# Kernel tuning notes

Measured on AMD Instinct MI355X. Metric: run time of the kernel, lower is better.

The kernel has to match this reference:

```python
import jax, jax.numpy as jnp
import numpy as np

B, R, C, NH, G = 32, 64, 96, 3, 8   # batch, patches_resolution, dim, heads, group(window) size
HD = C // NH                         # head dim = 32
SCALE = HD ** -0.5
HID = 4 * C                          # mlp hidden = mlp_ratio * dim


def setup_inputs() -> dict:
    key = jax.random.key(0)
    ks = jax.random.split(key, 16)
    n = jax.random.normal
    s = 0.02
    return {
        "x": n(ks[0], (B, R * R, C), jnp.float32),
        "w_qkv": n(ks[1], (C, 3 * C), jnp.float32) * s,
        "b_qkv": jnp.zeros((3 * C,), jnp.float32),
        "w_lepe": n(ks[2], (C, 1, 3, 3), jnp.float32) * s,  # depthwise conv, OIHW with groups=C
        "b_lepe": jnp.zeros((C,), jnp.float32),
        "w_proj": n(ks[3], (C, C), jnp.float32) * s,
        "b_proj": jnp.zeros((C,), jnp.float32),
        "g1": jnp.ones((C,), jnp.float32),
        "bt1": jnp.zeros((C,), jnp.float32),
        "g2": jnp.ones((C,), jnp.float32),
        "bt2": jnp.zeros((C,), jnp.float32),
        "w_fc1": n(ks[4], (C, HID), jnp.float32) * s,
        "b_fc1": jnp.zeros((HID,), jnp.float32),
        "w_fc2": n(ks[5], (HID, C), jnp.float32) * s,
        "b_fc2": jnp.zeros((C,), jnp.float32),
    }


def _ln(x, g, b):
    m = x.mean(-1, keepdims=True)
    v = ((x - m) ** 2).mean(-1, keepdims=True)
    return (x - m) * jax.lax.rsqrt(v + 1e-5) * g + b


def reference(x, w_qkv, b_qkv, w_lepe, b_lepe, w_proj, b_proj,
              g1, bt1, g2, bt2, w_fc1, b_fc1, w_fc2, b_fc2):
    Bn, L, _ = x.shape
    H = W = R
    shortcut = x
    # norm1 + SDA window partition: (B,H,W,C) -> (B*nW, G*G, C)
    h = _ln(x, g1, bt1).reshape(Bn, H // G, G, W // G, G, C)
    h = h.transpose(0, 1, 3, 2, 4, 5).reshape(-1, G * G, C)
    B_ = h.shape[0]
    qkv = (h @ w_qkv + b_qkv).reshape(B_, G * G, 3, NH, HD).transpose(2, 0, 3, 1, 4)
    q, k, v = qkv[0], qkv[1], qkv[2]            # (B_, NH, G*G, HD)
    # LePE: depthwise 3x3 conv on V viewed as (B_, C, G, G)
    vimg = v.transpose(0, 1, 3, 2).reshape(B_, C, G, G)
    lepe = jax.lax.conv_general_dilated(
        vimg, w_lepe, window_strides=(1, 1), padding='SAME',
        feature_group_count=C, dimension_numbers=('NCHW', 'OIHW', 'NCHW'))
    lepe = lepe + b_lepe[None, :, None, None]
    lepe = lepe.reshape(B_, NH, HD, G * G).transpose(0, 1, 3, 2)  # (B_, NH, G*G, HD)
    # attention (no mask registered in this block)
    attn = jax.nn.softmax((q * SCALE) @ k.transpose(0, 1, 3, 2), axis=-1)
    o = (attn @ v + lepe).transpose(0, 2, 1, 3).reshape(B_, G * G, C)
    o = o @ w_proj + b_proj
    # window reverse
    o = o.reshape(Bn, H // G, W // G, G, G, C).transpose(0, 1, 3, 2, 4, 5).reshape(Bn, L, C)
    x1 = shortcut + o
    # MLP block (exact GELU, as torch nn.GELU default)
    m = _ln(x1, g2, bt2)
    m = jax.nn.gelu(m @ w_fc1 + b_fc1, approximate=False) @ w_fc2 + b_fc2
    return (x1 + m, attn)
```

## Files before the change

### kernel.cpp

```cpp
#include <hip/hip_runtime.h>
#include <hip/hip_bf16.h>

typedef short short8 __attribute__((ext_vector_type(8)));
typedef float f32x4 __attribute__((ext_vector_type(4)));

constexpr int BDIM = 32, RDIM = 64, CDIM = 96, NH_ = 3, HD_ = 32;
constexpr int LTOK = RDIM * RDIM;
constexpr int GG = 64;
constexpr int HID = 384;
constexpr int NWIN = 2048;
constexpr float SCALE = 0.17677669529663687f;
constexpr long OUT1OFF = (long)BDIM * LTOK * CDIM;

constexpr int O_WQKVT = 0;
constexpr int O_WPROJT = 27648;
constexpr int O_WFC1T = 36864;
constexpr int O_WFC2T = 73728;
constexpr int W_TOT = 110592;

__device__ __forceinline__ unsigned short f2b(float f) {
  return __builtin_bit_cast(unsigned short, __float2bfloat16(f));
}
__device__ __forceinline__ float b2f(unsigned short u) {
  return __bfloat162float(__builtin_bit_cast(__hip_bfloat16, u));
}

__global__ void prep_weights(const float* __restrict__ wqkv,
                             const float* __restrict__ wproj,
                             const float* __restrict__ wfc1,
                             const float* __restrict__ wfc2,
                             unsigned short* __restrict__ ws) {
  int i = blockIdx.x * 256 + threadIdx.x;
  if (i >= W_TOT) return;
  float v;
  if (i < O_WPROJT) {
    int n = i / 96, k = i - n * 96;
    v = wqkv[k * 288 + n];
  } else if (i < O_WFC1T) {
    int j = i - O_WPROJT, n = j / 96, k = j - n * 96;
    v = wproj[k * 96 + n];
  } else if (i < O_WFC2T) {
    int j = i - O_WFC1T, n = j / 96, k = j - n * 96;
    v = wfc1[k * 384 + n];
  } else {
    int j = i - O_WFC2T, n = j / 384, k = j - n * 384;
    v = wfc2[k * 96 + n];
  }
  ws[i] = f2b(v);
}

__global__ __launch_bounds__(256, 2)
void attn_mfma(const float* __restrict__ x, const float* __restrict__ bqkv,
               const float* __restrict__ wlepe, const float* __restrict__ blepe,
               const float* __restrict__ bproj, const float* __restrict__ g1,
               const float* __restrict__ bt1,
               const unsigned short* __restrict__ ws, float* __restrict__ out) {
  constexpr int SA = 104;
  constexpr int SQ = 200;
  constexpr int SV = 72;
  constexpr int SP = 72;
  __shared__ __attribute__((aligned(16))) unsigned short hA[64 * SA];
  __shared__ __attribute__((aligned(16))) unsigned short qkS[64 * SQ];
  __shared__ __attribute__((aligned(16))) unsigned short vS[96 * SV];
  __shared__ __attribute__((aligned(16))) unsigned short pS[64 * SP];
  float* red = (float*)pS;

  const int tid = threadIdx.x, lane = tid & 63;
  const int wv = __builtin_amdgcn_readfirstlane(tid >> 6);
  const int w = blockIdx.x, b = w >> 6, wi = w & 63, wr = wi >> 3, wc = wi & 7;
  const long xbase = (long)b * (LTOK * CDIM);
  const int l15 = lane & 15, lk = (lane >> 4) * 8, lr = (lane >> 4) * 4;

  {
    const int tok = lane;
    const long rowbase =
        xbase + (long)((wr * 8 + (tok >> 3)) * RDIM + wc * 8 + (tok & 7)) * CDIM;
    float xv[24], s1 = 0.f, s2 = 0.f;
#pragma unroll
    for (int i = 0; i < 24; ++i) {
      float v = x[rowbase + wv * 24 + i];
      xv[i] = v; s1 += v; s2 += v * v;
    }
    red[wv * 64 + tok] = s1;
    red[256 + wv * 64 + tok] = s2;
    __syncthreads();
    float m = 0.f, vv = 0.f;
#pragma unroll
    for (int q = 0; q < 4; ++q) { m += red[q * 64 + tok]; vv += red[256 + q * 64 + tok]; }
    m *= (1.f / 96.f);
    vv = vv * (1.f / 96.f) - m * m;
    float rs = rsqrtf(vv + 1e-5f);
#pragma unroll
    for (int i = 0; i < 24; ++i) {
      int c = wv * 24 + i;
      hA[tok * SA + c] = f2b((xv[i] - m) * rs * g1[c] + bt1[c]);
    }
  }
  __syncthreads();

  {
    f32x4 acc[18];
#pragma unroll
    for (int t = 0; t < 18; ++t) acc[t] = (f32x4){0.f, 0.f, 0.f, 0.f};
    const int arow = wv * 16 + l15;
#pragma unroll
    for (int kk = 0; kk < 3; ++kk) {
      short8 a = *(const short8*)&hA[arow * SA + kk * 32 + lk];
#pragma unroll
      for (int nt = 0; nt < 18; ++nt) {
        short8 bw = *(const short8*)&ws[O_WQKVT + (nt * 16 + l15) * 96 + kk * 32 + lk];
        acc[nt] = __builtin_amdgcn_mfma_f32_16x16x32_bf16(a, bw, acc[nt], 0, 0, 0);
      }
    }
#pragma unroll
    for (int nt = 0; nt < 18; ++nt) {
      int n0 = nt * 16 + l15;
      float bias = bqkv[n0];
#pragma unroll
      for (int r = 0; r < 4; ++r) {
        int tk = wv * 16 + lr + r;
        float v = acc[nt][r] + bias;
        if (n0 < 96) qkS[tk * SQ + n0] = f2b(v * SCALE);
        else if (n0 < 192) qkS[tk * SQ + n0] = f2b(v);
        else vS[(n0 - 192) * SV + tk] = f2b(v);
      }
    }
  }
  __syncthreads();

  for (int h = 0; h < NH_; ++h) {
    f32x4 sacc[4];
#pragma unroll
    for (int t = 0; t < 4; ++t) sacc[t] = (f32x4){0.f, 0.f, 0.f, 0.f};
    short8 aq = *(const short8*)&qkS[(wv * 16 + l15) * SQ + h * 32 + lk];
#pragma unroll
    for (int nt = 0; nt < 4; ++nt) {
      short8 bk = *(const short8*)&qkS[(nt * 16 + l15) * SQ + 96 + h * 32 + lk];
      sacc[nt] = __builtin_amdgcn_mfma_f32_16x16x32_bf16(aq, bk, sacc[nt], 0, 0, 0);
    }
    float p[4][4];
#pragma unroll
    for (int r = 0; r < 4; ++r) {
      float mx = -1e30f;
#pragma unroll
      for (int nt = 0; nt < 4; ++nt) mx = fmaxf(mx, sacc[nt][r]);
#pragma unroll
      for (int s = 1; s < 16; s <<= 1) mx = fmaxf(mx, __shfl_xor(mx, s, 64));
      float sum = 0.f;
#pragma unroll
      for (int nt = 0; nt < 4; ++nt) {
        float e = __expf(sacc[nt][r] - mx);
        p[nt][r] = e; sum += e;
      }
#pragma unroll
      for (int s = 1; s < 16; s <<= 1) sum += __shfl_xor(sum, s, 64);
      float inv = 1.f / sum;
#pragma unroll
      for (int nt = 0; nt < 4; ++nt) p[nt][r] *= inv;
    }
    const long o1base = OUT1OFF + ((long)(w * NH_ + h) * GG) * GG;
#pragma unroll
    for (int nt = 0; nt < 4; ++nt) {
      int col = nt * 16 + l15;
#pragma unroll
      for (int r = 0; r < 4; ++r) {
        int row = wv * 16 + lr + r;
        out[o1base + (long)row * GG + col] = p[nt][r];
        pS[row * SP + col] = f2b(p[nt][r]);
      }
    }
    f32x4 oa[2];
    oa[0] = (f32x4){0.f, 0.f, 0.f, 0.f};
    oa[1] = (f32x4){0.f, 0.f, 0.f, 0.f};
#pragma unroll
    for (int kk = 0; kk < 2; ++kk) {
      short8 ap = *(const short8*)&pS[(wv * 16 + l15) * SP + kk * 32 + lk];
#pragma unroll
      for (int nt = 0; nt < 2; ++nt) {
        short8 bv = *(const short8*)&vS[(h * 32 + nt * 16 + l15) * SV + kk * 32 + lk];
        oa[nt] = __builtin_amdgcn_mfma_f32_16x16x32_bf16(ap, bv, oa[nt], 0, 0, 0);
      }
    }
#pragma unroll
    for (int nt = 0; nt < 2; ++nt) {
      int d = nt * 16 + l15, c = h * 32 + d;
      float lw9[9];
#pragma unroll
      for (int q = 0; q < 9; ++q) lw9[q] = wlepe[c * 9 + q];
      float lb = blepe[c];
#pragma unroll
      for (int r = 0; r < 4; ++r) {
        int tk = wv * 16 + lr + r;
        int tr_ = tk >> 3, tc_ = tk & 7;
        float a = lb;
#pragma unroll
        for (int kh = 0; kh < 3; ++kh)
#pragma unroll
          for (int kw2 = 0; kw2 < 3; ++kw2) {
            int rr = tr_ + kh - 1, cc = tc_ + kw2 - 1;
            if (rr >= 0 && rr < 8 && cc >= 0 && cc < 8)
              a += lw9[kh * 3 + kw2] * b2f(vS[c * SV + rr * 8 + cc]);
          }
        hA[tk * SA + c] = f2b(oa[nt][r] + a);
      }
    }
  }
  __syncthreads();

  {
    f32x4 pacc[6];
#pragma unroll
    for (int t = 0; t < 6; ++t) pacc[t] = (f32x4){0.f, 0.f, 0.f, 0.f};
#pragma unroll
    for (int kk = 0; kk < 3; ++kk) {
      short8 ao = *(const short8*)&hA[(wv * 16 + l15) * SA + kk * 32 + lk];
#pragma unroll
      for (int nt = 0; nt < 6; ++nt) {
        short8 bw = *(const short8*)&ws[O_WPROJT + (nt * 16 + l15) * 96 + kk * 32 + lk];
        pacc[nt] = __builtin_amdgcn_mfma_f32_16x16x32_bf16(ao, bw, pacc[nt], 0, 0, 0);
      }
    }
#pragma unroll
    for (int nt = 0; nt < 6; ++nt) {
      int ch = nt * 16 + l15;
      float bias = bproj[ch];
#pragma unroll
      for (int r = 0; r < 4; ++r) {
        int tk = wv * 16 + lr + r;
        long g = xbase + (long)((wr * 8 + (tk >> 3)) * RDIM + wc * 8 + (tk & 7)) * CDIM + ch;
        out[g] = x[g] + pacc[nt][r] + bias;
      }
    }
  }
}

__global__ __launch_bounds__(256, 2)
void mlp_mfma(const float* __restrict__ bfc1, const float* __restrict__ bfc2,
              const float* __restrict__ g2, const float* __restrict__ bt2,
              const unsigned short* __restrict__ ws, float* __restrict__ out) {
  constexpr int SB = 104, SH = 392;
  __shared__ __attribute__((aligned(16))) unsigned short hB[64 * SB];
  __shared__ __attribute__((aligned(16))) unsigned short Hs[64 * SH];
  float* red = (float*)Hs;

  const int tid = threadIdx.x, lane = tid & 63;
  const int wv = __builtin_amdgcn_readfirstlane(tid >> 6);
  const long t0 = (long)blockIdx.x * GG;
  const int l15 = lane & 15, lk = (lane >> 4) * 8, lr = (lane >> 4) * 4;

  {
    const int tok = lane;
    const long rb = (t0 + tok) * CDIM;
    float xv[24], s1 = 0.f, s2 = 0.f;
#pragma unroll
    for (int i = 0; i < 24; ++i) {
      float v = out[rb + wv * 24 + i];
      xv[i] = v; s1 += v; s2 += v * v;
    }
    red[wv * 64 + tok] = s1;
    red[256 + wv * 64 + tok] = s2;
    __syncthreads();
    float m = 0.f, vv = 0.f;
#pragma unroll
    for (int q = 0; q < 4; ++q) { m += red[q * 64 + tok]; vv += red[256 + q * 64 + tok]; }
    m *= (1.f / 96.f);
    vv = vv * (1.f / 96.f) - m * m;
    float rs = rsqrtf(vv + 1e-5f);
#pragma unroll
    for (int i = 0; i < 24; ++i) {
      int c = wv * 24 + i;
      hB[tok * SB + c] = f2b((xv[i] - m) * rs * g2[c] + bt2[c]);
    }
  }
  __syncthreads();

  for (int half = 0; half < 2; ++half) {
    f32x4 acc[12];
#pragma unroll
    for (int t = 0; t < 12; ++t) acc[t] = (f32x4){0.f, 0.f, 0.f, 0.f};
#pragma unroll
    for (int kk = 0; kk < 3; ++kk) {
      short8 a = *(const short8*)&hB[(wv * 16 + l15) * SB + kk * 32 + lk];
#pragma unroll
      for (int nt = 0; nt < 12; ++nt) {
        int n = half * 192 + nt * 16 + l15;
        short8 bw = *(const short8*)&ws[O_WFC1T + n * 96 + kk * 32 + lk];
        acc[nt] = __builtin_amdgcn_mfma_f32_16x16x32_bf16(a, bw, acc[nt], 0, 0, 0);
      }
    }
#pragma unroll
    for (int nt = 0; nt < 12; ++nt) {
      int n = half * 192 + nt * 16 + l15;
      float bias = bfc1[n];
#pragma unroll
      for (int r = 0; r < 4; ++r) {
        int tk = wv * 16 + lr + r;
        float v = acc[nt][r] + bias;
        float gl = 0.5f * v * (1.f + erff(v * 0.70710678118654752f));
        Hs[tk * SH + n] = f2b(gl);
      }
    }
  }
  __syncthreads();

  {
    f32x4 acc[6];
#pragma unroll
    for (int t = 0; t < 6; ++t) acc[t] = (f32x4){0.f, 0.f, 0.f, 0.f};
#pragma unroll
    for (int kk = 0; kk < 12; ++kk) {
      short8 a = *(const short8*)&Hs[(wv * 16 + l15) * SH + kk * 32 + lk];
#pragma unroll
      for (int nt = 0; nt < 6; ++nt) {
        short8 bw = *(const short8*)&ws[O_WFC2T + (nt * 16 + l15) * 384 + kk * 32 + lk];
        acc[nt] = __builtin_amdgcn_mfma_f32_16x16x32_bf16(a, bw, acc[nt], 0, 0, 0);
      }
    }
#pragma unroll
    for (int nt = 0; nt < 6; ++nt) {
      int ch = nt * 16 + l15;
      float bias = bfc2[ch];
#pragma unroll
      for (int r = 0; r < 4; ++r) {
        int tk = wv * 16 + lr + r;
        long g = (t0 + tk) * CDIM + ch;
        out[g] = out[g] + acc[nt][r] + bias;
      }
    }
  }
}

struct PF {
  const float *x, *w_qkv, *b_qkv, *w_lepe, *b_lepe, *w_proj, *b_proj;
  const float *g1, *bt1, *g2, *bt2, *w_fc1, *b_fc1, *w_fc2, *b_fc2;
  float* out;
};

__global__ __launch_bounds__(256, 2)
void attn_scalar(PF p) {
  constexpr int SA = 66;
  __shared__ __hip_bfloat16 bufA[CDIM * SA];
  __shared__ __hip_bfloat16 qkvT[288 * GG];
  __shared__ __hip_bfloat16 sPad[GG * SA];
  __shared__ float meanS[GG], rstdS[GG];

  const int w = blockIdx.x;
  const int b = w >> 6, wi = w & 63, wr = wi >> 3, wc = wi & 7;
  const int tid = threadIdx.x, lane = tid & 63;
  const int wv = __builtin_amdgcn_readfirstlane(tid >> 6);
  const long xbase = (long)b * (LTOK * CDIM);

  for (int k = 0; k < 24; ++k) {
    int e = tid + k * 256, wrow = e / 768, o = e - wrow * 768;
    int tir = o / 96, ch = o - tir * 96;
    long g = xbase + ((wr * 8 + wrow) * RDIM + wc * 8 + tir) * CDIM + ch;
    bufA[ch * SA + wrow * 8 + tir] = __float2bfloat16(p.x[g]);
  }
  __syncthreads();
  if (wv == 0) {
    float m = 0.f;
    for (int c = 0; c < CDIM; ++c) m += __bfloat162float(bufA[c * SA + lane]);
    m *= (1.f / CDIM);
    float var = 0.f;
    for (int c = 0; c < CDIM; ++c) {
      float d = __bfloat162float(bufA[c * SA + lane]) - m;
      var += d * d;
    }
    meanS[lane] = m;
    rstdS[lane] = rsqrtf(var * (1.f / CDIM) + 1e-5f);
  }
  __syncthreads();
  {
    float m = meanS[lane], rs = rstdS[lane];
    for (int cc = 0; cc < 24; ++cc) {
      int c = wv * 24 + cc;
      float v = __bfloat162float(bufA[c * SA + lane]);
      bufA[c * SA + lane] = __float2bfloat16((v - m) * rs * p.g1[c] + p.bt1[c]);
    }
  }
  __syncthreads();
  for (int tile = 0; tile < 2; ++tile) {
    int j0 = wv * 72 + tile * 36;
    float acc[36];
#pragma unroll
    for (int jj = 0; jj < 36; ++jj) acc[jj] = p.b_qkv[j0 + jj];
#pragma unroll 1
    for (int c = 0; c < CDIM; ++c) {
      float hv = __bfloat162float(bufA[c * SA + lane]);
#pragma unroll
      for (int jj = 0; jj < 36; ++jj) acc[jj] += hv * p.w_qkv[c * 288 + j0 + jj];
    }
#pragma unroll
    for (int jj = 0; jj < 36; ++jj)
      qkvT[(j0 + jj) * GG + lane] = __float2bfloat16(acc[jj]);
  }
  __syncthreads();
  for (int hh = 0; hh < NH_; ++hh) {
    float kreg[HD_];
#pragma unroll
    for (int d = 0; d < HD_; ++d)
      kreg[d] = __bfloat162float(qkvT[(CDIM + hh * HD_ + d) * GG + lane]);
#pragma unroll 1
    for (int r = 0; r < 16; ++r) {
      int i = wv * 16 + r;
      float acc = 0.f;
#pragma unroll
      for (int d = 0; d < HD_; ++d)
        acc += __bfloat162float(qkvT[(hh * HD_ + d) * GG + i]) * kreg[d];
      sPad[lane * SA + i] = __float2bfloat16(acc * SCALE);
    }
#pragma unroll 1
    for (int r = 0; r < 16; ++r) {
      int i = wv * 16 + r;
      float v = __bfloat162float(sPad[lane * SA + i]);
      float mx = v;
#pragma unroll
      for (int s = 32; s > 0; s >>= 1) mx = fmaxf(mx, __shfl_xor(mx, s, 64));
      float e = __expf(v - mx);
      float sum = e;
#pragma unroll
      for (int s = 32; s > 0; s >>= 1) sum += __shfl_xor(sum, s, 64);
      float rr = e / sum;
      sPad[lane * SA + i] = __float2bfloat16(rr);
      p.out[OUT1OFF + ((long)(w * NH_ + hh) * GG + i) * GG + lane] = rr;
    }
    __syncthreads();
    {
      int d0 = wv * 8;
      float acc[8];
#pragma unroll
      for (int dd = 0; dd < 8; ++dd) acc[dd] = 0.f;
#pragma unroll 1
      for (int j = 0; j < GG; ++j) {
        float sv = __bfloat162float(sPad[j * SA + lane]);
#pragma unroll
        for (int dd = 0; dd < 8; ++dd)
          acc[dd] += sv * __bfloat162float(qkvT[(2 * CDIM + hh * HD_ + d0 + dd) * GG + j]);
      }
      int tr = lane >> 3, tc = lane & 7;
#pragma unroll
      for (int dd = 0; dd < 8; ++dd) {
        int c = hh * HD_ + d0 + dd;
        float a = p.b_lepe[c];
#pragma unroll
        for (int kh = 0; kh < 3; ++kh)
#pragma unroll
          for (int kw = 0; kw < 3; ++kw) {
            int rr2 = tr + kh - 1, cc2 = tc + kw - 1;
            if (rr2 >= 0 && rr2 < 8 && cc2 >= 0 && cc2 < 8)
              a += p.w_lepe[c * 9 + kh * 3 + kw] *
                   __bfloat162float(qkvT[(2 * CDIM + hh * HD_ + d0 + dd) * GG + rr2 * 8 + cc2]);
          }
        acc[dd] += a;
      }
#pragma unroll
      for (int dd = 0; dd < 8; ++dd)
        bufA[(hh * HD_ + d0 + dd) * SA + lane] = __float2bfloat16(acc[dd]);
    }
    __syncthreads();
  }
  __hip_bfloat16* projT = qkvT;
  {
    int j0 = wv * 24;
    float acc[24];
#pragma unroll
    for (int jj = 0; jj < 24; ++jj) acc[jj] = p.b_proj[j0 + jj];
#pragma unroll 1
    for (int c = 0; c < CDIM; ++c) {
      float ov = __bfloat162float(bufA[c * SA + lane]);
#pragma unroll
      for (int jj = 0; jj < 24; ++jj) acc[jj] += ov * p.w_proj[c * CDIM + j0 + jj];
    }
#pragma unroll
    for (int jj = 0; jj < 24; ++jj)
      projT[(j0 + jj) * SA + lane] = __float2bfloat16(acc[jj]);
  }
  __syncthreads();
  for (int k = 0; k < 24; ++k) {
    int e = tid + k * 256, wrow = e / 768, o = e - wrow * 768;
    int tir = o / 96, ch = o - tir * 96;
    long g = xbase + ((wr * 8 + wrow) * RDIM + wc * 8 + tir) * CDIM + ch;
    p.out[g] = p.x[g] + __bfloat162float(projT[ch * SA + wrow * 8 + tir]);
  }
}

__global__ __launch_bounds__(256, 2)
void mlp_scalar(PF p) {
  constexpr int SB = 66;
  __shared__ __hip_bfloat16 bufB[CDIM * SB];
  __shared__ __hip_bfloat16 hidT[HID * GG];
  __shared__ float meanS[GG], rstdS[GG];

  const int tid = threadIdx.x, lane = tid & 63;
  const int wv = __builtin_amdgcn_readfirstlane(tid >> 6);
  const long t0 = (long)blockIdx.x * GG;

  for (int k = 0; k < 24; ++k) {
    int e = tid + k * 256, tok = e / 96, ch = e - tok * 96;
    bufB[ch * SB + tok] = __float2bfloat16(p.out[(t0 + tok) * CDIM + ch]);
  }
  __syncthreads();
  if (wv == 0) {
    float m = 0.f;
    for (int c = 0; c < CDIM; ++c) m += __bfloat162float(bufB[c * SB + lane]);
    m *= (1.f / CDIM);
    float var = 0.f;
    for (int c = 0; c < CDIM; ++c) {
      float d = __bfloat162float(bufB[c * SB + lane]) - m;
      var += d * d;
    }
    meanS[lane] = m;
    rstdS[lane] = rsqrtf(var * (1.f / CDIM) + 1e-5f);
  }
  __syncthreads();
  {
    float m = meanS[lane], rs = rstdS[lane];
    for (int cc = 0; cc < 24; ++cc) {
      int c = wv * 24 + cc;
      float v = __bfloat162float(bufB[c * SB + lane]);
      bufB[c * SB + lane] = __float2bfloat16((v - m) * rs * p.g2[c] + p.bt2[c]);
    }
  }
  __syncthreads();
  for (int tile = 0; tile < 4; ++tile) {
    int j0 = wv * 96 + tile * 24;
    float acc[24];
#pragma unroll
    for (int jj = 0; jj < 24; ++jj) acc[jj] = p.b_fc1[j0 + jj];
#pragma unroll 1
    for (int c = 0; c < CDIM; ++c) {
      float hv = __bfloat162float(bufB[c * SB + lane]);
#pragma unroll
      for (int jj = 0; jj < 24; ++jj) acc[jj] += hv * p.w_fc1[c * HID + j0 + jj];
    }
#pragma unroll
    for (int jj = 0; jj < 24; ++jj) {
      float xg = acc[jj];
      hidT[(j0 + jj) * GG + lane] =
          __float2bfloat16(0.5f * xg * (1.f + erff(xg * 0.70710678118f)));
    }
  }
  __syncthreads();
  {
    int j0 = wv * 24;
    float acc[24];
#pragma unroll
    for (int jj = 0; jj < 24; ++jj) acc[jj] = p.b_fc2[j0 + jj];
#pragma unroll 1
    for (int h = 0; h < HID; ++h) {
      float hv = __bfloat162float(hidT[h * GG + lane]);
#pragma unroll
      for (int jj = 0; jj < 24; ++jj) acc[jj] += hv * p.w_fc2[h * CDIM + j0 + jj];
    }
#pragma unroll
    for (int jj = 0; jj < 24; ++jj)
      bufB[(j0 + jj) * SB + lane] = __float2bfloat16(acc[jj]);
  }
  __syncthreads();
  for (int k = 0; k < 24; ++k) {
    int e = tid + k * 256, tok = e / 96, ch = e - tok * 96;
    long g = (t0 + tok) * CDIM + ch;
    p.out[g] = p.out[g] + __bfloat162float(bufB[ch * SB + tok]);
  }
}

extern "C" void kernel_launch(void* const* d_in, const int* in_sizes, int n_in,
                              void* d_out, int out_size, void* d_ws, size_t ws_size,
                              hipStream_t stream) {
  const float* x = (const float*)d_in[0];
  const float* w_qkv = (const float*)d_in[1];
  const float* b_qkv = (const float*)d_in[2];
  const float* w_lepe = (const float*)d_in[3];
  const float* b_lepe = (const float*)d_in[4];
  const float* w_proj = (const float*)d_in[5];
  const float* b_proj = (const float*)d_in[6];
  const float* g1 = (const float*)d_in[7];
  const float* bt1 = (const float*)d_in[8];
  const float* g2 = (const float*)d_in[9];
  const float* bt2 = (const float*)d_in[10];
  const float* w_fc1 = (const float*)d_in[11];
  const float* b_fc1 = (const float*)d_in[12];
  const float* w_fc2 = (const float*)d_in[13];
  const float* b_fc2 = (const float*)d_in[14];
  float* out = (float*)d_out;
  const int mlp_blocks = (BDIM * LTOK) / GG;

  if (ws_size >= (size_t)W_TOT * sizeof(unsigned short)) {
    unsigned short* ws = (unsigned short*)d_ws;
    prep_weights<<<(W_TOT + 255) / 256, 256, 0, stream>>>(w_qkv, w_proj, w_fc1, w_fc2, ws);
    attn_mfma<<<NWIN, 256, 0, stream>>>(x, b_qkv, w_lepe, b_lepe, b_proj, g1, bt1, ws, out);
    mlp_mfma<<<mlp_blocks, 256, 0, stream>>>(b_fc1, b_fc2, g2, bt2, ws, out);
  } else {
    PF p{x, w_qkv, b_qkv, w_lepe, b_lepe, w_proj, b_proj,
         g1, bt1, g2, bt2, w_fc1, b_fc1, w_fc2, b_fc2, out};
    attn_scalar<<<NWIN, 256, 0, stream>>>(p);
    mlp_scalar<<<mlp_blocks, 256, 0, stream>>>(p);
  }
}
```

Baseline: 426.7 us.

## Fuse MLP hidden chunks into fc2 and use a polynomial erf for GELU

Restructures the MLP kernel so each wave computes fc1 in chunks of 96 hidden units, applies GELU, and immediately accumulates into fc2. The full 384-wide hidden tile no longer sits in LDS, and occupancy is raised to 4 blocks per SM. LayerNorm stats are now reduced with wave shuffles and vectorized loads instead of an LDS reduction and barriers. GELU uses the Abramowitz–Stegun erf approximation with fast rcp and exp instead of erff, which costs some accuracy.

```diff
diff --git a/kernel.cpp b/kernel.cpp
--- a/kernel.cpp
+++ b/kernel.cpp
@@ -23,6 +23,20 @@
 }
 __device__ __forceinline__ float b2f(unsigned short u) {
   return __bfloat162float(__builtin_bit_cast(__hip_bfloat16, u));
+}
+
+__device__ __forceinline__ float gelu_f(float x) {
+  float u = x * 0.70710678118654752f;
+  float ax = __builtin_fabsf(u);
+  float t = __builtin_amdgcn_rcpf(1.f + 0.3275911f * ax);
+  float poly = t * (0.254829592f +
+               t * (-0.284496736f +
+               t * (1.421413741f +
+               t * (-1.453152027f +
+               t * 1.061405429f))));
+  float erf_abs = 1.f - poly * __expf(-ax * ax);
+  float erf_u = (u < 0.f) ? -erf_abs : erf_abs;
+  return 0.5f * x * (1.f + erf_u);
 }
 
 __global__ void prep_weights(const float* __restrict__ wqkv,
@@ -234,98 +248,99 @@
   }
 }
 
-__global__ __launch_bounds__(256, 2)
+__global__ __launch_bounds__(256, 4)
 void mlp_mfma(const float* __restrict__ bfc1, const float* __restrict__ bfc2,
               const float* __restrict__ g2, const float* __restrict__ bt2,
               const unsigned short* __restrict__ ws, float* __restrict__ out) {
-  constexpr int SB = 104, SH = 392;
+  constexpr int SB = 104;
+  constexpr int SHQ = 104;
   __shared__ __attribute__((aligned(16))) unsigned short hB[64 * SB];
-  __shared__ __attribute__((aligned(16))) unsigned short Hs[64 * SH];
-  float* red = (float*)Hs;
+  __shared__ __attribute__((aligned(16))) unsigned short Hq[64 * SHQ];
 
   const int tid = threadIdx.x, lane = tid & 63;
   const int wv = __builtin_amdgcn_readfirstlane(tid >> 6);
   const long t0 = (long)blockIdx.x * GG;
   const int l15 = lane & 15, lk = (lane >> 4) * 8, lr = (lane >> 4) * 4;
-
-  {
-    const int tok = lane;
-    const long rb = (t0 + tok) * CDIM;
+  const int p = lane >> 4;
+  const int tok = wv * 16 + l15;
+
+  {
+    const float* rb = out + (t0 + tok) * CDIM + p * 24;
     float xv[24], s1 = 0.f, s2 = 0.f;
 #pragma unroll
+    for (int i = 0; i < 6; ++i) {
+      f32x4 v4 = *(const f32x4*)(rb + i * 4);
+#pragma unroll
+      for (int j = 0; j < 4; ++j) {
+        float v = v4[j];
+        xv[i * 4 + j] = v; s1 += v; s2 += v * v;
+      }
+    }
+    s1 += __shfl_xor(s1, 16, 64); s1 += __shfl_xor(s1, 32, 64);
+    s2 += __shfl_xor(s2, 16, 64); s2 += __shfl_xor(s2, 32, 64);
+    float m = s1 * (1.f / 96.f);
+    float vv = s2 * (1.f / 96.f) - m * m;
+    float rs = rsqrtf(vv + 1e-5f);
+    unsigned short tmp[24];
+#pragma unroll
     for (int i = 0; i < 24; ++i) {
-      float v = out[rb + wv * 24 + i];
-      xv[i] = v; s1 += v; s2 += v * v;
-    }
-    red[wv * 64 + tok] = s1;
-    red[256 + wv * 64 + tok] = s2;
-    __syncthreads();
-    float m = 0.f, vv = 0.f;
-#pragma unroll
-    for (int q = 0; q < 4; ++q) { m += red[q * 64 + tok]; vv += red[256 + q * 64 + tok]; }
-    m *= (1.f / 96.f);
-    vv = vv * (1.f / 96.f) - m * m;
-    float rs = rsqrtf(vv + 1e-5f);
-#pragma unroll
-    for (int i = 0; i < 24; ++i) {
-      int c = wv * 24 + i;
-      hB[tok * SB + c] = f2b((xv[i] - m) * rs * g2[c] + bt2[c]);
-    }
-  }
-  __syncthreads();
-
-  for (int half = 0; half < 2; ++half) {
-    f32x4 acc[12];
-#pragma unroll
-    for (int t = 0; t < 12; ++t) acc[t] = (f32x4){0.f, 0.f, 0.f, 0.f};
+      int c = p * 24 + i;
+      tmp[i] = f2b((xv[i] - m) * rs * g2[c] + bt2[c]);
+    }
+#pragma unroll
+    for (int i = 0; i < 3; ++i)
+      *(short8*)&hB[tok * SB + p * 24 + i * 8] = *(const short8*)&tmp[i * 8];
+  }
+
+  f32x4 acc2[6];
+#pragma unroll
+  for (int t = 0; t < 6; ++t) acc2[t] = (f32x4){0.f, 0.f, 0.f, 0.f};
+
+#pragma unroll 1
+  for (int q = 0; q < 4; ++q) {
+    f32x4 acc1[6];
+#pragma unroll
+    for (int t = 0; t < 6; ++t) acc1[t] = (f32x4){0.f, 0.f, 0.f, 0.f};
 #pragma unroll
     for (int kk = 0; kk < 3; ++kk) {
       short8 a = *(const short8*)&hB[(wv * 16 + l15) * SB + kk * 32 + lk];
 #pragma unroll
-      for (int nt = 0; nt < 12; ++nt) {
-        int n = half * 192 + nt * 16 + l15;
+      for (int nt = 0; nt < 6; ++nt) {
+        int n = q * 96 + nt * 16 + l15;
         short8 bw = *(const short8*)&ws[O_WFC1T + n * 96 + kk * 32 + lk];
-        acc[nt] = __builtin_amdgcn_mfma_f32_16x16x32_bf16(a, bw, acc[nt], 0, 0, 0);
-      }
-    }
-#pragma unroll
-    for (int nt = 0; nt < 12; ++nt) {
-      int n = half * 192 + nt * 16 + l15;
+        acc1[nt] = __builtin_amdgcn_mfma_f32_16x16x32_bf16(a, bw, acc1[nt], 0, 0, 0);
+      }
+    }
+#pragma unroll
+    for (int nt = 0; nt < 6; ++nt) {
+      int n = q * 96 + nt * 16 + l15;
       float bias = bfc1[n];
 #pragma unroll
       for (int r = 0; r < 4; ++r) {
         int tk = wv * 16 + lr + r;
-        float v = acc[nt][r] + bias;
-        float gl = 0.5f * v * (1.f + erff(v * 0.70710678118654752f));
-        Hs[tk * SH + n] = f2b(gl);
-      }
-    }
-  }
-  __syncthreads();
-
-  {
-    f32x4 acc[6];
-#pragma unroll
-    for (int t = 0; t < 6; ++t) acc[t] = (f32x4){0.f, 0.f, 0.f, 0.f};
-#pragma unroll
-    for (int kk = 0; kk < 12; ++kk) {
-      short8 a = *(const short8*)&Hs[(wv * 16 + l15) * SH + kk * 32 + lk];
+        Hq[tk * SHQ + nt * 16 + l15] = f2b(gelu_f(acc1[nt][r] + bias));
+      }
+    }
+#pragma unroll
+    for (int kk = 0; kk < 3; ++kk) {
+      short8 a = *(const short8*)&Hq[(wv * 16 + l15) * SHQ + kk * 32 + lk];
 #pragma unroll
       for (int nt = 0; nt < 6; ++nt) {
-        short8 bw = *(const short8*)&ws[O_WFC2T + (nt * 16 + l15) * 384 + kk * 32 + lk];
-        acc[nt] = __builtin_amdgcn_mfma_f32_16x16x32_bf16(a, bw, acc[nt], 0, 0, 0);
-      }
-    }
-#pragma unroll
-    for (int nt = 0; nt < 6; ++nt) {
-      int ch = nt * 16 + l15;
-      float bias = bfc2[ch];
-#pragma unroll
-      for (int r = 0; r < 4; ++r) {
-        int tk = wv * 16 + lr + r;
-        long g = (t0 + tk) * CDIM + ch;
-        out[g] = out[g] + acc[nt][r] + bias;
-      }
+        short8 bw = *(const short8*)&ws[O_WFC2T + (nt * 16 + l15) * 384 + q * 96 + kk * 32 + lk];
+        acc2[nt] = __builtin_amdgcn_mfma_f32_16x16x32_bf16(a, bw, acc2[nt], 0, 0, 0);
+      }
+    }
+  }
+
+#pragma unroll
+  for (int nt = 0; nt < 6; ++nt) {
+    int ch = nt * 16 + l15;
+    float bias = bfc2[ch];
+#pragma unroll
+    for (int r = 0; r < 4; ++r) {
+      int tk = wv * 16 + lr + r;
+      long g = (t0 + tk) * CDIM + ch;
+      out[g] = out[g] + acc2[nt][r] + bias;
     }
   }
 }
```

Result: faster. 405.5 us (-5.0%).
